# Optimization experiments

Hardware: AMD Instinct MI355X
Metric: run time of the kernel (lower is better)

Reference implementation:

```python
import jax, jax.numpy as jnp
import numpy as np
from jax import lax

B, G = 8, 64
V = G * G * G  # 262144, matches fc1 in-features


def setup_inputs() -> dict:
    key = jax.random.key(0)
    ks = jax.random.split(key, 10)
    boundary = (jax.random.uniform(ks[0], (B, 1, G, G, G)) < 0.1).astype(jnp.float32)
    conv1_w = jax.random.normal(ks[1], (64, 1, 3, 3, 3), jnp.float32) * 0.1
    conv1_b = jax.random.normal(ks[2], (64,), jnp.float32) * 0.01
    conv2_w = jax.random.normal(ks[3], (1, 64, 3, 3, 3), jnp.float32) * 0.05
    conv2_b = jax.random.normal(ks[4], (1,), jnp.float32) * 0.01
    fc1_w = jax.random.normal(ks[5], (256, V), jnp.float32) * (1.0 / np.sqrt(V))
    fc1_b = jax.random.normal(ks[6], (256,), jnp.float32) * 0.01
    fc2_w = jax.random.normal(ks[7], (1, 256), jnp.float32) * (1.0 / 16.0)
    fc2_b = jax.random.normal(ks[8], (1,), jnp.float32) * 0.01
    noise = jax.random.uniform(ks[9], (B, V), jnp.float32)
    return {"boundary": boundary, "conv1_w": conv1_w, "conv1_b": conv1_b,
            "conv2_w": conv2_w, "conv2_b": conv2_b, "fc1_w": fc1_w,
            "fc1_b": fc1_b, "fc2_w": fc2_w, "fc2_b": fc2_b,
            "noise": noise, "num_points": 10}


def _conv3d(x, w, b):
    # NCDHW / OIDHW, stride 1, padding 1 with k=3 -> SAME
    y = lax.conv_general_dilated(x, w, (1, 1, 1), 'SAME',
                                 dimension_numbers=('NCDHW', 'OIDHW', 'NCDHW'))
    return y + b[None, :, None, None, None]


def _generate_points(boundary, noise, num_points):
    # Vectorized equivalent of the per-point rejection loop:
    # uniform sampling without replacement over cells where boundary == 0.
    bflat = boundary.reshape(boundary.shape[0], -1)  # [B, V]
    scores = jnp.where(bflat > 0.5, -jnp.inf, noise)
    _, idx = lax.top_k(scores, num_points)  # [B, k]
    rows = jnp.arange(bflat.shape[0])[:, None]
    pts = jnp.zeros_like(bflat).at[rows, idx].set(1.0)
    return pts.reshape(boundary.shape)


def reference(boundary, conv1_w, conv1_b, conv2_w, conv2_b,
              fc1_w, fc1_b, fc2_w, fc2_b, noise, num_points):
    x = jax.nn.relu(_conv3d(boundary, conv1_w, conv1_b))
    x = jax.nn.relu(_conv3d(x, conv2_w, conv2_b))
    x = x.reshape(x.shape[0], -1)                      # [B, V]
    x = jax.nn.relu(x @ fc1_w.T + fc1_b)               # [B, 256]
    probability = jax.nn.sigmoid(x @ fc2_w.T + fc2_b) * 100.0  # [B, 1]
    points = _generate_points(boundary, noise, num_points)
    return points, probability
```

## Files before the change

### kernel.cpp

```cpp
#include <hip/hip_runtime.h>
#include <math.h>

#define G 64
#define GV (G*G*G)
#define NB 8
#define NP 9

typedef unsigned char u8;
typedef unsigned short u16;
typedef unsigned int u32;
typedef unsigned long long U64;
typedef __bf16 bf16x8 __attribute__((ext_vector_type(8)));
typedef float f32x4 __attribute__((ext_vector_type(4)));
typedef unsigned short u16x4 __attribute__((ext_vector_type(4)));

union BF8 { u16 s[8]; bf16x8 v; };

__device__ __forceinline__ float bf2f(u16 h) {
    union { u32 u; float f; } c; c.u = ((u32)h) << 16; return c.f;
}
__device__ __forceinline__ u16 f2bf(float f) {
    union { float f; u32 u; } c; c.f = f;
    u32 u = c.u;
    return (u16)((u + 0x7fffu + ((u >> 16) & 1u)) >> 16);
}
__device__ __forceinline__ u32 cvt_pk_bf16(float lo, float hi) {
    u32 r;
    asm volatile("v_cvt_pk_bf16_f32 %0, %1, %2" : "=v"(r) : "v"(lo), "v"(hi));
    return r;
}

#define YSTRIDE 36
#define BPB 32
#define IDXM 0x3FFFFu
#define POOLB 40448

__global__ __launch_bounds__(256, 4) void convA_topk_kernel(
    const float* __restrict__ bnd,
    const float* __restrict__ w1, const float* __restrict__ b1,
    const float* __restrict__ w2,
    u16* __restrict__ zbuf,
    const float* __restrict__ noise,
    U64* __restrict__ cand, float4* __restrict__ pts_out)
{
    __shared__ __align__(16) char pool[POOLB];
    int tid = threadIdx.x;

    if (blockIdx.x < 256) {
        int blk = blockIdx.x & 31;
        int b   = blockIdx.x >> 5;
        int vbase = blk * (GV / BPB);

        float4* zp = pts_out + ((size_t)b * GV + vbase) / 4;
#pragma unroll
        for (int i = 0; i < 8; i++)
            zp[i * 256 + tid] = make_float4(0.f, 0.f, 0.f, 0.f);

        const float* bd = bnd + (size_t)b * GV + vbase;
        const float* nz = noise + (size_t)b * GV + vbase;

        U64 top[10];
#pragma unroll
        for (int k = 0; k < 10; k++) top[k] = 0ull;

        for (int i = 0; i < (GV / BPB) / 256; i++) {
            int e = i * 256 + tid;
            float bv = bd[e];
            float s  = nz[e];
            U64 p = (bv > 0.5f) ? 0ull
                  : ((((U64)__float_as_uint(s)) << 32) |
                     (IDXM - (unsigned)(vbase + e)));
            if (p > top[9]) {
#pragma unroll
                for (int k = 0; k < 10; k++) {
                    U64 mx = p > top[k] ? p : top[k];
                    U64 mn = p > top[k] ? top[k] : p;
                    top[k] = mx; p = mn;
                }
            }
        }

        U64* lcand = (U64*)pool;
        U64* rv    = (U64*)(pool + 20480);
        int* rp    = (int*)(pool + 22528);
#pragma unroll
        for (int k = 0; k < 10; k++) lcand[tid * 10 + k] = top[k];
        __syncthreads();

        for (int pass = 0; pass < 10; pass++) {
            U64 bv = 0; int bp = 0;
            for (int i = tid; i < 2560; i += 256) {
                U64 xv = lcand[i];
                if (xv > bv) { bv = xv; bp = i; }
            }
            rv[tid] = bv; rp[tid] = bp;
            __syncthreads();
            for (int off = 128; off > 0; off >>= 1) {
                if (tid < off) {
                    if (rv[tid + off] > rv[tid]) { rv[tid] = rv[tid + off]; rp[tid] = rp[tid + off]; }
                }
                __syncthreads();
            }
            if (tid == 0) {
                cand[((size_t)b * BPB + blk) * 10 + pass] = rv[0];
                lcand[rp[0]] = 0ull;
            }
            __syncthreads();
        }
        return;
    }

    int bid = blockIdx.x - 256;
    int box = bid & 255, b = bid >> 8;
    const float* bd = bnd + (size_t)b * GV;
    u16* zb = zbuf + (size_t)b * (NP * (size_t)GV);

    u8*  halo8 = (u8*)pool;
    u32* ybase = (u32*)(pool + 2384);

    int z0 = (box >> 4) * 4, y0 = (box & 15) * 4;

    {
        float* ldsW = (float*)ybase;
        for (int i = tid; i < 3520; i += 256) {
            float v;
            if (i < 1728)      v = w1[i];
            else if (i < 3456) v = w2[i - 1728];
            else               v = b1[i - 3456];
            ldsW[i] = v;
        }
    }

    for (int i = tid; i < 2378; i += 256) {
        u8 hval = 0;
        if (i < 2376) {
            int hz = i / 396, rem = i - hz * 396;
            int hy = rem / 66, hx = rem - hy * 66;
            int gz = z0 + hz - 1, gy = y0 + hy - 1, gx = hx - 1;
            if (((unsigned)gz < (unsigned)G) & ((unsigned)gy < (unsigned)G) &
                ((unsigned)gx < (unsigned)G)) {
                float f = bd[(gz << 12) + (gy << 6) + gx];
                hval = (f > 0.5f) ? (u8)1 : (u8)0;
            }
        }
        halo8[i] = hval;
    }

    __syncthreads();

    int wv = tid >> 6, lane = tid & 63;
    int g = lane >> 4, lr = lane & 15;

    const float* ldsW = (const float*)ybase;
    BF8 w1A[4];
#pragma unroll
    for (int m = 0; m < 4; m++) {
        int c = 16 * m + lr;
#pragma unroll
        for (int j = 0; j < 8; j++) {
            int kk = 8 * g + j;
            float w = (kk < 27) ? ldsW[c * 27 + kk] : 0.0f;
            w1A[m].s[j] = f2bf(w);
        }
    }
    BF8 w2dx[3][2];
#pragma unroll
    for (int dx = 0; dx < 3; dx++)
#pragma unroll
        for (int ks = 0; ks < 2; ks++)
#pragma unroll
            for (int j = 0; j < 8; j++) {
                int ch = 32 * ks + 8 * g + j;
                float w = (lr < NP) ? ldsW[1728 + ch * 27 + 3 * lr + dx] : 0.0f;
                w2dx[dx][ks].s[j] = f2bf(w);
            }
    float bias[4][4];
#pragma unroll
    for (int m = 0; m < 4; m++)
#pragma unroll
        for (int r = 0; r < 4; r++) bias[m][r] = ldsW[3456 + 16 * m + 4 * g + r];

    int tapoff[8];
#pragma unroll
    for (int j = 0; j < 8; j++) {
        int kk = 8 * g + j;
        int kc = kk < 27 ? kk : 0;
        int dz = kc / 9, ry = kc - dz * 9;
        int dy = ry / 3, dxx = ry - dy * 3;
        tapoff[j] = dz * 396 + dy * 66 + dxx;
    }

    __syncthreads();

    u32* myY = ybase + wv * (66 * YSTRIDE);

    for (int li = 0; li < 4; li++) {
        int l = wv * 4 + li;
        int zl = l >> 2, yl = l & 3;
        int linebase = (zl * 6 + yl) * 66 + lr;
        int vbase = ((z0 + zl) << 12) + ((y0 + yl) << 6);

        myY[(lane < 32 ? 0 : 65 * YSTRIDE) + (lane & 31)] = 0;

        for (int xt = 0; xt < 4; xt++) {
            int x0 = xt * 16;
            BF8 xB;
#pragma unroll
            for (int j = 0; j < 8; j++) {
                u16 f = (u16)halo8[linebase + x0 + tapoff[j]];
                xB.s[j] = (u16)(f * 0x3F80u);
            }

            f32x4 yac[4];
#pragma unroll
            for (int m = 0; m < 4; m++) {
                f32x4 c0;
                c0[0] = bias[m][0]; c0[1] = bias[m][1];
                c0[2] = bias[m][2]; c0[3] = bias[m][3];
                yac[m] = __builtin_amdgcn_mfma_f32_16x16x32_bf16(
                    w1A[m].v, xB.v, c0, 0, 0, 0);
            }

            int rx = x0 + lr + 1;
#pragma unroll
            for (int m = 0; m < 4; m++) {
                float a0 = fmaxf(yac[m][0], 0.f), a1 = fmaxf(yac[m][1], 0.f);
                float a2 = fmaxf(yac[m][2], 0.f), a3 = fmaxf(yac[m][3], 0.f);
                u32 h01 = cvt_pk_bf16(a0, a1);
                u32 h23 = cvt_pk_bf16(a2, a3);
                *(U64*)&myY[rx * YSTRIDE + 8 * m + 2 * g] =
                    (U64)h01 | ((U64)h23 << 32);
            }
        }

        asm volatile("" ::: "memory");

        for (int xt = 0; xt < 4; xt++) {
            int x0 = xt * 16;
            f32x4 zac = f32x4{0.f, 0.f, 0.f, 0.f};
#pragma unroll
            for (int dx = 0; dx < 3; dx++) {
                int rbase = (x0 + lr + dx) * YSTRIDE;
#pragma unroll
                for (int ks = 0; ks < 2; ks++) {
                    bf16x8 yB = *(const bf16x8*)&myY[rbase + 16 * ks + 4 * g];
                    zac = __builtin_amdgcn_mfma_f32_16x16x32_bf16(
                        w2dx[dx][ks].v, yB, zac, 0, 0, 0);
                }
            }

            int vg = vbase + x0 + lr;
#pragma unroll
            for (int r = 0; r < 4; r++) {
                int p = 4 * g + r;
                if (p < NP) {
                    u32 pk = cvt_pk_bf16(zac[r], zac[r]);
                    zb[(size_t)p * GV + vg] = (u16)pk;
                }
            }
        }

        asm volatile("" ::: "memory");
    }
}

__global__ __launch_bounds__(256) void convB_topk2_kernel(
    const u16* __restrict__ zbuf,
    u16* __restrict__ xout,
    const float* __restrict__ b2,
    const U64* __restrict__ cand, float* __restrict__ pts)
{
    int tid = threadIdx.x;

    if (blockIdx.x < 8) {
        int b = blockIdx.x;
        __shared__ U64 lc[BPB * 10];
        __shared__ U64 rv[256];
        __shared__ int rp[256];
        __shared__ int widx[10];
        for (int i = tid; i < BPB * 10; i += 256) lc[i] = cand[(size_t)b * BPB * 10 + i];
        __syncthreads();

        for (int pass = 0; pass < 10; pass++) {
            U64 bv = 0; int bp = 0;
            for (int i = tid; i < BPB * 10; i += 256) {
                U64 xv = lc[i];
                if (xv > bv) { bv = xv; bp = i; }
            }
            rv[tid] = bv; rp[tid] = bp;
            __syncthreads();
            for (int off = 128; off > 0; off >>= 1) {
                if (tid < off) {
                    if (rv[tid + off] > rv[tid]) { rv[tid] = rv[tid + off]; rp[tid] = rp[tid + off]; }
                }
                __syncthreads();
            }
            if (tid == 0) { widx[pass] = (int)(IDXM - (u32)(rv[0] & 0xffffffffu)); lc[rp[0]] = 0ull; }
            __syncthreads();
        }
        if (tid < 10) pts[(size_t)b * GV + widx[tid]] = 1.0f;
        return;
    }

    int r = blockIdx.x - 8;
    int vblk = r & 127, b = r >> 7;
    const u16* zb = zbuf + (size_t)b * (NP * (size_t)GV);
    u16* xo = xout + (size_t)b * GV;

    int t8 = vblk * 256 + tid;
    int v0 = t8 * 8;
    int zc = v0 >> 12, yc = (v0 >> 6) & 63, x0 = v0 & 63;

    float bb = b2[0];
    float acc[8];
#pragma unroll
    for (int i = 0; i < 8; i++) acc[i] = bb;

#pragma unroll
    for (int dz = 0; dz < 3; dz++)
#pragma unroll
    for (int dy = 0; dy < 3; dy++) {
        int p = dz * 3 + dy;
        int zz = zc + dz - 1, yy = yc + dy - 1;
        bool ok = ((unsigned)zz < (unsigned)G) & ((unsigned)yy < (unsigned)G);
        if (ok) {
            const uint4* src = (const uint4*)(zb + (size_t)p * GV +
                                              (zz << 12) + (yy << 6) + x0);
            uint4 d = *src;
            u32 w[4] = {d.x, d.y, d.z, d.w};
#pragma unroll
            for (int q = 0; q < 4; q++) {
                acc[2 * q]     += bf2f((u16)(w[q] & 0xffffu));
                acc[2 * q + 1] += bf2f((u16)(w[q] >> 16));
            }
        }
    }

    uint4 o;
    o.x = cvt_pk_bf16(fmaxf(acc[0], 0.f), fmaxf(acc[1], 0.f));
    o.y = cvt_pk_bf16(fmaxf(acc[2], 0.f), fmaxf(acc[3], 0.f));
    o.z = cvt_pk_bf16(fmaxf(acc[4], 0.f), fmaxf(acc[5], 0.f));
    o.w = cvt_pk_bf16(fmaxf(acc[6], 0.f), fmaxf(acc[7], 0.f));
    *(uint4*)(xo + v0) = o;
}

__global__ __launch_bounds__(256) void fc1_kernel(
    const float* __restrict__ W, const u16* __restrict__ x,
    float* __restrict__ pacc)
{
    int bid = blockIdx.x;
    int xcd  = bid & 7;
    int slot = bid >> 3;
    int vc = (xcd << 3) | (slot >> 5);
    int jt = slot & 31;
    int tid = threadIdx.x;
    int j0 = jt * 8;
    size_t v0 = (size_t)vc * 4096;

    const f32x4* Wp[8];
#pragma unroll
    for (int jj = 0; jj < 8; jj++)
        Wp[jj] = reinterpret_cast<const f32x4*>(W + (size_t)(j0 + jj) * GV + v0);
    const u16* Xp[NB];
#pragma unroll
    for (int b = 0; b < NB; b++)
        Xp[b] = x + (size_t)b * GV + v0;

    float acc[8][NB];
#pragma unroll
    for (int jj = 0; jj < 8; jj++)
#pragma unroll
        for (int b = 0; b < NB; b++) acc[jj][b] = 0.0f;

    for (int i = 0; i < 4; i++) {
        int e = i * 256 + tid;
        f32x4 wvv[8];
#pragma unroll
        for (int jj = 0; jj < 8; jj++)
            wvv[jj] = __builtin_nontemporal_load(&Wp[jj][e]);
        f32x4 xv[NB];
#pragma unroll
        for (int b = 0; b < NB; b++) {
            u16x4 xr = *(const u16x4*)(Xp[b] + e * 4);
            xv[b][0] = bf2f(xr[0]); xv[b][1] = bf2f(xr[1]);
            xv[b][2] = bf2f(xr[2]); xv[b][3] = bf2f(xr[3]);
        }
#pragma unroll
        for (int b = 0; b < NB; b++) {
#pragma unroll
            for (int jj = 0; jj < 8; jj++) {
                acc[jj][b] = fmaf(wvv[jj][0], xv[b][0], acc[jj][b]);
                acc[jj][b] = fmaf(wvv[jj][1], xv[b][1], acc[jj][b]);
                acc[jj][b] = fmaf(wvv[jj][2], xv[b][2], acc[jj][b]);
                acc[jj][b] = fmaf(wvv[jj][3], xv[b][3], acc[jj][b]);
            }
        }
    }

    __shared__ float sacc[256][36];
    __shared__ float p2[8][40];
#pragma unroll
    for (int pass = 0; pass < 2; pass++) {
        if (pass > 0) __syncthreads();
        float4* row = reinterpret_cast<float4*>(&sacc[tid][0]);
#pragma unroll
        for (int jj = 0; jj < 4; jj++) {
            int js = pass * 4 + jj;
            row[jj * 2 + 0] = make_float4(acc[js][0], acc[js][1], acc[js][2], acc[js][3]);
            row[jj * 2 + 1] = make_float4(acc[js][4], acc[js][5], acc[js][6], acc[js][7]);
        }
        __syncthreads();
        {
            int o = tid & 31, gg = tid >> 5;
            float s = 0.0f;
#pragma unroll
            for (int k = 0; k < 32; k++) s += sacc[gg * 32 + k][o];
            p2[gg][o] = s;
        }
        __syncthreads();
        if (tid < 32) {
            float s = 0.0f;
#pragma unroll
            for (int gg = 0; gg < 8; gg++) s += p2[gg][tid];
            int jj = tid >> 3, b = tid & 7;
            pacc[((size_t)b * 64 + vc) * 256 + (j0 + pass * 4 + jj)] = s;
        }
    }
}

__global__ __launch_bounds__(256) void fc_final_kernel(
    const float* __restrict__ pacc, const float* __restrict__ fc1_b,
    const float* __restrict__ fc2_w, const float* __restrict__ fc2_b,
    float* __restrict__ prob)
{
    int j = threadIdx.x;
    float h[NB];
#pragma unroll
    for (int b = 0; b < NB; b++) h[b] = 0.0f;
    for (int c = 0; c < 64; c++) {
#pragma unroll
        for (int b = 0; b < NB; b++)
            h[b] += pacc[((size_t)b * 64 + c) * 256 + j];
    }
    float w2j = fc2_w[j];
    float contrib[NB];
#pragma unroll
    for (int b = 0; b < NB; b++)
        contrib[b] = fmaxf(h[b] + fc1_b[j], 0.0f) * w2j;

    int lane = j & 63, wid = j >> 6;
#pragma unroll
    for (int b = 0; b < NB; b++)
#pragma unroll
        for (int off = 32; off > 0; off >>= 1)
            contrib[b] += __shfl_down(contrib[b], off, 64);

    __shared__ float sred[4][NB];
    if (lane == 0) {
#pragma unroll
        for (int b = 0; b < NB; b++) sred[wid][b] = contrib[b];
    }
    __syncthreads();
    if (j < NB) {
        float t = sred[0][j] + sred[1][j] + sred[2][j] + sred[3][j] + fc2_b[0];
        prob[j] = 100.0f / (1.0f + expf(-t));
    }
}

extern "C" void kernel_launch(void* const* d_in, const int* in_sizes, int n_in,
                              void* d_out, int out_size, void* d_ws, size_t ws_size,
                              hipStream_t stream)
{
    const float* bnd   = (const float*)d_in[0];
    const float* w1    = (const float*)d_in[1];
    const float* b1    = (const float*)d_in[2];
    const float* w2    = (const float*)d_in[3];
    const float* b2    = (const float*)d_in[4];
    const float* fw1   = (const float*)d_in[5];
    const float* fb1   = (const float*)d_in[6];
    const float* fw2   = (const float*)d_in[7];
    const float* fb2   = (const float*)d_in[8];
    const float* noise = (const float*)d_in[9];

    float* out = (float*)d_out;
    char* ws = (char*)d_ws;

    const size_t xbuf_off = 0;
    const size_t pacc_off = xbuf_off + (size_t)NB * GV * 2;
    const size_t cand_off = pacc_off + (size_t)NB * 64 * 256 * 4;
    const size_t zbuf_off = cand_off + (size_t)NB * BPB * 10 * 8;

    u16*   xbuf = (u16*)(ws + xbuf_off);
    float* pacc = (float*)(ws + pacc_off);
    U64*   cand = (U64*)(ws + cand_off);
    u16*   zbuf = (u16*)(ws + zbuf_off);

    convA_topk_kernel<<<2304, 256, 0, stream>>>(bnd, w1, b1, w2, zbuf,
                                                noise, cand, (float4*)out);

    convB_topk2_kernel<<<1032, 256, 0, stream>>>(zbuf, xbuf, b2, cand, out);

    fc1_kernel<<<2048, 256, 0, stream>>>(fw1, xbuf, pacc);

    fc_final_kernel<<<1, 256, 0, stream>>>(pacc, fb1, fw2, fb2,
                                           out + (size_t)NB * GV);
}
```

Measured before the change: 140.3 us.

## Fuse final FC reduction into fc1 via last-block atomic counter

Removes the separate single-block fc_final kernel launch. The last fc1 block to finish, detected through an atomic counter that convB resets, performs the cross-chunk reduction, ReLU, fc2 and sigmoid. It also changes the conv halo tap loads to 32-bit word reads with bit extraction instead of byte loads. The gain is one fewer launch and less launch gap, at the cost of threadfences and an atomic in every fc1 block.

```diff
diff --git a/kernel.cpp b/kernel.cpp
--- a/kernel.cpp
+++ b/kernel.cpp
@@ -116,6 +116,7 @@
     u16* zb = zbuf + (size_t)b * (NP * (size_t)GV);
 
     u8*  halo8 = (u8*)pool;
+    u32* haloW = (u32*)pool;
     u32* ybase = (u32*)(pool + 2384);
 
     int z0 = (box >> 4) * 4, y0 = (box & 15) * 4;
@@ -207,8 +208,10 @@
             BF8 xB;
 #pragma unroll
             for (int j = 0; j < 8; j++) {
-                u16 f = (u16)halo8[linebase + x0 + tapoff[j]];
-                xB.s[j] = (u16)(f * 0x3F80u);
+                int a = linebase + x0 + tapoff[j];
+                u32 word = haloW[a >> 2];
+                u32 bit = (word >> ((a & 3) * 8)) & 1u;
+                xB.s[j] = (u16)(bit ? 0x3F80u : 0u);
             }
 
             f32x4 yac[4];
@@ -268,7 +271,8 @@
     const u16* __restrict__ zbuf,
     u16* __restrict__ xout,
     const float* __restrict__ b2,
-    const U64* __restrict__ cand, float* __restrict__ pts)
+    const U64* __restrict__ cand, float* __restrict__ pts,
+    u32* __restrict__ fc_cnt)
 {
     int tid = threadIdx.x;
 
@@ -303,6 +307,8 @@
     }
 
     int r = blockIdx.x - 8;
+    if (r == 0 && tid == 0) *fc_cnt = 0;
+
     int vblk = r & 127, b = r >> 7;
     const u16* zb = zbuf + (size_t)b * (NP * (size_t)GV);
     u16* xo = xout + (size_t)b * GV;
@@ -346,7 +352,9 @@
 
 __global__ __launch_bounds__(256) void fc1_kernel(
     const float* __restrict__ W, const u16* __restrict__ x,
-    float* __restrict__ pacc)
+    float* __restrict__ pacc, u32* __restrict__ fc_cnt,
+    const float* __restrict__ fc1_b, const float* __restrict__ fc2_w,
+    const float* __restrict__ fc2_b, float* __restrict__ prob)
 {
     int bid = blockIdx.x;
     int xcd  = bid & 7;
@@ -426,14 +434,15 @@
             pacc[((size_t)b * 64 + vc) * 256 + (j0 + pass * 4 + jj)] = s;
         }
     }
-}
-
-__global__ __launch_bounds__(256) void fc_final_kernel(
-    const float* __restrict__ pacc, const float* __restrict__ fc1_b,
-    const float* __restrict__ fc2_w, const float* __restrict__ fc2_b,
-    float* __restrict__ prob)
-{
-    int j = threadIdx.x;
+
+    __threadfence();
+    __shared__ int slast;
+    if (tid == 0) slast = (atomicAdd(fc_cnt, 1u) == 2047u) ? 1 : 0;
+    __syncthreads();
+    if (!slast) return;
+    __threadfence();
+
+    int j = tid;
     float h[NB];
 #pragma unroll
     for (int b = 0; b < NB; b++) h[b] = 0.0f;
@@ -455,14 +464,15 @@
         for (int off = 32; off > 0; off >>= 1)
             contrib[b] += __shfl_down(contrib[b], off, 64);
 
-    __shared__ float sred[4][NB];
+    float* sred = &p2[0][0];
     if (lane == 0) {
 #pragma unroll
-        for (int b = 0; b < NB; b++) sred[wid][b] = contrib[b];
+        for (int b = 0; b < NB; b++) sred[wid * NB + b] = contrib[b];
     }
     __syncthreads();
     if (j < NB) {
-        float t = sred[0][j] + sred[1][j] + sred[2][j] + sred[3][j] + fc2_b[0];
+        float t = sred[0 * NB + j] + sred[1 * NB + j] + sred[2 * NB + j] +
+                  sred[3 * NB + j] + fc2_b[0];
         prob[j] = 100.0f / (1.0f + expf(-t));
     }
 }
@@ -488,20 +498,22 @@
     const size_t xbuf_off = 0;
     const size_t pacc_off = xbuf_off + (size_t)NB * GV * 2;
     const size_t cand_off = pacc_off + (size_t)NB * 64 * 256 * 4;
-    const size_t zbuf_off = cand_off + (size_t)NB * BPB * 10 * 8;
+    const size_t cnt_off  = cand_off + (size_t)NB * BPB * 10 * 8;
+    const size_t zbuf_off = cnt_off + 256;
 
     u16*   xbuf = (u16*)(ws + xbuf_off);
     float* pacc = (float*)(ws + pacc_off);
     U64*   cand = (U64*)(ws + cand_off);
+    u32*   fcnt = (u32*)(ws + cnt_off);
     u16*   zbuf = (u16*)(ws + zbuf_off);
 
     convA_topk_kernel<<<2304, 256, 0, stream>>>(bnd, w1, b1, w2, zbuf,
                                                 noise, cand, (float4*)out);
 
-    convB_topk2_kernel<<<1032, 256, 0, stream>>>(zbuf, xbuf, b2, cand, out);
-
-    fc1_kernel<<<2048, 256, 0, stream>>>(fw1, xbuf, pacc);
-
-    fc_final_kernel<<<1, 256, 0, stream>>>(pacc, fb1, fw2, fb2,
-                                           out + (size_t)NB * GV);
-}
+    convB_topk2_kernel<<<1032, 256, 0, stream>>>(zbuf, xbuf, b2, cand, out,
+                                                 fcnt);
+
+    fc1_kernel<<<2048, 256, 0, stream>>>(fw1, xbuf, pacc, fcnt,
+                                         fb1, fw2, fb2,
+                                         out + (size_t)NB * GV);
+}
```

Result: slower. 454.0 us (+223.6%).
